# Optimization experiments

Hardware: AMD Instinct MI355X
Metric: run time of the kernel (lower is better)

## Reference

```python
import jax, jax.numpy as jnp
import numpy as np

D_IN = 1024
D_OUT = 1024
CTX_LEN = 2048
BATCH = 4
SEQ = 2048


def setup_inputs() -> dict:
    key = jax.random.key(0)
    kx, kq, kk, kv = jax.random.split(key, 4)
    x = jax.random.normal(kx, (BATCH, SEQ, D_IN), dtype=jnp.float32)
    s = 1.0 / np.sqrt(D_IN)
    # torch nn.Linear weight is (d_out, d_in); store transposed for x @ W
    W_q = jax.random.uniform(kq, (D_IN, D_OUT), dtype=jnp.float32, minval=-s, maxval=s)
    W_k = jax.random.uniform(kk, (D_IN, D_OUT), dtype=jnp.float32, minval=-s, maxval=s)
    W_v = jax.random.uniform(kv, (D_IN, D_OUT), dtype=jnp.float32, minval=-s, maxval=s)
    return {"x": x, "W_q": W_q, "W_k": W_k, "W_v": W_v}


def reference(x, W_q, W_k, W_v):
    b, n, _ = x.shape
    d_out = W_q.shape[1]
    q = x @ W_q            # [b, n, d_out]
    k = x @ W_k
    v = x @ W_v
    scores = jnp.einsum('bqd,bkd->bqk', q, k)  # [b, n, n]
    causal = jnp.triu(jnp.ones((n, n), dtype=bool), k=1)
    scores = jnp.where(causal, -jnp.inf, scores)
    attn = jax.nn.softmax(scores / jnp.sqrt(jnp.float32(d_out)), axis=-1)
    # dropout p=0.0 -> identity
    return jnp.einsum('bqk,bkd->bqd', attn, v)
```

## Files before the change

kernel.cpp:

```cpp
#include <hip/hip_runtime.h>
#include <hip/hip_bf16.h>

#define BATCH 4
#define SEQ   2048
#define DIN   1024
#define DOUT  1024
#define N3    3072
#define MTOT  (BATCH*SEQ)

typedef __hip_bfloat16 bf16;
typedef __attribute__((ext_vector_type(8))) short bf16x8;
typedef __attribute__((ext_vector_type(4))) float f32x4;

#define MFMA(a,b,c) __builtin_amdgcn_mfma_f32_16x16x32_bf16(a,b,c,0,0,0)

union pack4 { bf16 h[4]; uint2 u2; };
union pack8 { bf16 h[8]; bf16x8 v; };

__device__ __forceinline__ void gl16(const bf16* g, bf16* l)
{
    __builtin_amdgcn_global_load_lds(
        (const __attribute__((address_space(1))) void*)g,
        (__attribute__((address_space(3))) void*)l, 16, 0, 0);
}


__global__ __launch_bounds__(256)
void k_prep(const float* __restrict__ x, const float* __restrict__ Wq,
            const float* __restrict__ Wk, const float* __restrict__ Wv,
            bf16* __restrict__ xb, bf16* __restrict__ Wt)
{
    __shared__ bf16 t[64][68];
    const int bid = blockIdx.x;
    if (bid < 8192) {
        long i = ((long)bid * 256 + threadIdx.x) * 4;
        float4 v = *(const float4*)(x + i);
        pack4 o;
        o.h[0] = __float2bfloat16(v.x);
        o.h[1] = __float2bfloat16(v.y);
        o.h[2] = __float2bfloat16(v.z);
        o.h[3] = __float2bfloat16(v.w);
        *(uint2*)(xb + i) = o.u2;
        return;
    }
    const int idx = bid - 8192;
    const int mat = idx >> 8;
    const int rem = idx & 255;
    const int k0 = (rem >> 4) * 64, n0 = (rem & 15) * 64;
    const float* W = (mat == 0) ? Wq : ((mat == 1) ? Wk : Wv);
#pragma unroll
    for (int p = 0; p < 4; ++p) {
        int kr = p * 16 + (threadIdx.x >> 4);
        int c4 = (threadIdx.x & 15) * 4;
        float4 v = *(const float4*)&W[(long)(k0 + kr) * DOUT + n0 + c4];
        t[c4 + 0][kr] = __float2bfloat16(v.x);
        t[c4 + 1][kr] = __float2bfloat16(v.y);
        t[c4 + 2][kr] = __float2bfloat16(v.z);
        t[c4 + 3][kr] = __float2bfloat16(v.w);
    }
    __syncthreads();
    bf16* O = Wt + (long)mat * DIN * DOUT;
#pragma unroll
    for (int i = 0; i < 2; ++i) {
        int l = threadIdx.x + i * 256;
        int n = l >> 3, c8 = (l & 7) * 8;
        pack8 o;
#pragma unroll
        for (int j = 0; j < 8; ++j) o.h[j] = t[n][c8 + j];
        *(bf16x8*)&O[(long)(n0 + n) * DIN + k0 + c8] = o.v;
    }
}


__device__ __forceinline__ void gemm_core(
    const bf16* __restrict__ Ab, long lda,
    const bf16* __restrict__ Bb, long ldb,
    int nk, bf16* __restrict__ As, bf16* __restrict__ Bs,
    f32x4 acc[4][4])
{
    const int tid  = threadIdx.x;
    const int lane = tid & 63;
    const int wave = tid >> 6;
    const int wm = (wave >> 1) * 64;
    const int wn = (wave & 1) * 64;
    const int r  = lane & 15;
    const int qd = lane >> 4;

    const int row0 = tid >> 3;
    const int c    = (tid & 7) ^ (row0 & 7);
    const long aoff = (long)row0 * lda + c * 8;
    const long boff = (long)row0 * ldb + c * 8;
    const long astep = 32 * lda, bstep = 32 * ldb;
    bf16* dA = &As[tid * 8];
    bf16* dB = &Bs[tid * 8];

    for (int kk = 0; kk < nk; ++kk) {
        const bf16* A = Ab + kk * 64 + aoff;
        const bf16* B = Bb + kk * 64 + boff;
#pragma unroll
        for (int i = 0; i < 4; ++i) {
            gl16(A + i * astep, dA + i * 2048);
            gl16(B + i * bstep, dB + i * 2048);
        }
        __syncthreads();
#pragma unroll
        for (int ks = 0; ks < 2; ++ks) {
            const int slot = ((ks * 4 + qd) ^ (r & 7)) * 8;
            bf16x8 af[4], bv[4];
#pragma unroll
            for (int mi = 0; mi < 4; ++mi)
                af[mi] = *(const bf16x8*)&As[(wm + mi * 16 + r) * 64 + slot];
#pragma unroll
            for (int ni = 0; ni < 4; ++ni)
                bv[ni] = *(const bf16x8*)&Bs[(wn + ni * 16 + r) * 64 + slot];
#pragma unroll
            for (int mi = 0; mi < 4; ++mi)
#pragma unroll
                for (int ni = 0; ni < 4; ++ni)
                    acc[mi][ni] = MFMA(af[mi], bv[ni], acc[mi][ni]);
        }
        __syncthreads();
    }
}


__global__ __launch_bounds__(256)
void k_gemm_qkv(const bf16* __restrict__ xb, const bf16* __restrict__ Wt,
                bf16* __restrict__ QK, bf16* __restrict__ Vt)
{
    __shared__ __align__(16) bf16 smem[17408];
    bf16* As = smem;
    bf16* Bs = smem + 8192;
    const int m0 = blockIdx.y * 128, n0 = blockIdx.x * 128;
    f32x4 acc[4][4] = {};
    gemm_core(xb + (long)m0 * DIN, DIN, Wt + (long)n0 * DIN, DIN, DIN / 64, As, Bs, acc);

    const int tid = threadIdx.x;
    const int lane = tid & 63, wave = tid >> 6;
    const int wm = (wave >> 1) * 64, wn = (wave & 1) * 64;
    const int r = lane & 15, qd = lane >> 4;

    if (n0 < 2048) {
#pragma unroll
        for (int mi = 0; mi < 4; ++mi)
#pragma unroll
            for (int ni = 0; ni < 4; ++ni)
#pragma unroll
                for (int j = 0; j < 4; ++j) {
                    int row = m0 + wm + mi * 16 + qd * 4 + j;
                    int col = n0 + wn + ni * 16 + r;
                    QK[(long)row * 2048 + col] = __float2bfloat16(acc[mi][ni][j]);
                }
    } else {
        const int ld = 136;
        bf16* T = smem;
#pragma unroll
        for (int mi = 0; mi < 4; ++mi)
#pragma unroll
            for (int ni = 0; ni < 4; ++ni) {
                pack4 p;
#pragma unroll
                for (int j = 0; j < 4; ++j) p.h[j] = __float2bfloat16(acc[mi][ni][j]);
                int d_l = wn + ni * 16 + r;
                int s_l = wm + mi * 16 + qd * 4;
                *(uint2*)&T[d_l * ld + s_l] = p.u2;
            }
        __syncthreads();
        const int n0v = n0 - 2048;
        const int bb = m0 >> 11;
        const int s0 = m0 & 2047;
        bf16* Ob = Vt + (long)bb * DOUT * SEQ + s0;
#pragma unroll
        for (int p = 0; p < 8; ++p) {
            int l = tid + p * 256;
            int d = l >> 4, s8 = (l & 15) * 8;
            bf16x8 vv = *(const bf16x8*)&T[d * ld + s8];
            *(bf16x8*)&Ob[(long)(n0v + d) * SEQ + s8] = vv;
        }
    }
}


__global__ __launch_bounds__(256, 3)
void k_gemm_scores(const bf16* __restrict__ QK, bf16* __restrict__ P,
                   float* __restrict__ rowSum)
{
    const int b = blockIdx.z, qt = blockIdx.y, kt = blockIdx.x;
    if (kt > qt) return;
    __shared__ __align__(16) bf16 As[128 * 64];
    __shared__ __align__(16) bf16 Bs[128 * 64];
    const bf16* A  = QK + (long)b * SEQ * 2048;
    const bf16* Bt = A + 1024;
    f32x4 acc[4][4] = {};
    gemm_core(A + (long)qt * 128 * 2048, 2048, Bt + (long)kt * 128 * 2048, 2048,
              DIN / 64, As, Bs, acc);

    bf16* Pb = P + (long)b * SEQ * SEQ;
    float* RS = rowSum + b * SEQ;
    const int lane = threadIdx.x & 63, wave = threadIdx.x >> 6;
    const int wm = (wave >> 1) * 64, wn = (wave & 1) * 64;
    const int r = lane & 15, qd = lane >> 4;

    float rp[4][4];
#pragma unroll
    for (int mi = 0; mi < 4; ++mi)
#pragma unroll
        for (int j = 0; j < 4; ++j) rp[mi][j] = 0.f;

#pragma unroll
    for (int mi = 0; mi < 4; ++mi)
#pragma unroll
        for (int ni = 0; ni < 4; ++ni)
#pragma unroll
            for (int j = 0; j < 4; ++j) {
                int row = qt * 128 + wm + mi * 16 + qd * 4 + j;
                int col = kt * 128 + wn + ni * 16 + r;
                float e = (col > row) ? 0.f : __expf(acc[mi][ni][j] * 0.03125f);
                rp[mi][j] += e;
                Pb[(long)row * SEQ + col] = __float2bfloat16(e);
            }
#pragma unroll
    for (int d = 1; d < 16; d <<= 1)
#pragma unroll
        for (int mi = 0; mi < 4; ++mi)
#pragma unroll
            for (int j = 0; j < 4; ++j)
                rp[mi][j] += __shfl_xor(rp[mi][j], d, 64);
    if (r == 0) {
#pragma unroll
        for (int mi = 0; mi < 4; ++mi)
#pragma unroll
            for (int j = 0; j < 4; ++j) {
                int row = qt * 128 + wm + mi * 16 + qd * 4 + j;
                atomicAdd(&RS[row], rp[mi][j]);
            }
    }
}


__global__ __launch_bounds__(256, 3)
void k_gemm_pv(const bf16* __restrict__ P, const bf16* __restrict__ Vt,
               const float* __restrict__ rowSum, float* __restrict__ O)
{
    const int b = blockIdx.z, nt = blockIdx.x;
    const int qt = (SEQ / 128 - 1) - blockIdx.y;
    __shared__ __align__(16) bf16 As[128 * 64];
    __shared__ __align__(16) bf16 Bs[128 * 64];
    const bf16* A  = P + (long)b * SEQ * SEQ + (long)qt * 128 * SEQ;
    const bf16* Bt = Vt + (long)b * DOUT * SEQ;
    const int nk = (qt + 1) * 2;
    f32x4 acc[4][4] = {};
    gemm_core(A, SEQ, Bt + (long)nt * 128 * SEQ, SEQ, nk, As, Bs, acc);

    float* Ob = O + (long)b * SEQ * DOUT;
    const float* RS = rowSum + b * SEQ;
    const int lane = threadIdx.x & 63, wave = threadIdx.x >> 6;
    const int wm = (wave >> 1) * 64, wn = (wave & 1) * 64;
    const int r = lane & 15, qd = lane >> 4;
#pragma unroll
    for (int mi = 0; mi < 4; ++mi)
#pragma unroll
        for (int j = 0; j < 4; ++j) {
            int row = qt * 128 + wm + mi * 16 + qd * 4 + j;
            float inv = 1.0f / RS[row];
#pragma unroll
            for (int ni = 0; ni < 4; ++ni) {
                int col = nt * 128 + wn + ni * 16 + r;
                Ob[(long)row * DOUT + col] = acc[mi][ni][j] * inv;
            }
        }
}


extern "C" void kernel_launch(void* const* d_in, const int* in_sizes, int n_in,
                              void* d_out, int out_size, void* d_ws, size_t ws_size,
                              hipStream_t stream)
{
    const float* x  = (const float*)d_in[0];
    const float* Wq = (const float*)d_in[1];
    const float* Wk = (const float*)d_in[2];
    const float* Wv = (const float*)d_in[3];
    float* out = (float*)d_out;

    char* ws = (char*)d_ws;
    bf16*  xb = (bf16*)(ws);
    bf16*  Wt = (bf16*)(ws + 16777216);
    bf16*  QK = (bf16*)(ws + 23068672);
    bf16*  Vt = (bf16*)(ws + 56623104);
    bf16*  P  = (bf16*)(ws + 73400320);
    float* RS = (float*)(ws + 106954752);

    hipMemsetAsync(RS, 0, BATCH * SEQ * sizeof(float), stream);
    k_prep<<<dim3(8192 + 768), 256, 0, stream>>>(x, Wq, Wk, Wv, xb, Wt);
    k_gemm_qkv<<<dim3(N3 / 128, MTOT / 128), 256, 0, stream>>>(xb, Wt, QK, Vt);
    k_gemm_scores<<<dim3(SEQ / 128, SEQ / 128, BATCH), 256, 0, stream>>>(QK, P, RS);
    k_gemm_pv<<<dim3(DOUT / 128, SEQ / 128, BATCH), 256, 0, stream>>>(P, Vt, RS, out);
}
```

Before: 223.3 us.

## Rewrite QKV projection GEMM as 128x256 tile, 8-wave pipelined kernel

Replaces the QKV GEMM with a 512-thread kernel on 128x256 tiles. It double-buffers LDS with async global-to-LDS loads, interleaved across two half-iterations, and raises wave priority around the MFMA bursts. The aim is to hide global load latency behind MFMA work and halve the number of blocks so each loaded tile is reused more. In exchange it uses about 96KB of LDS per block and hand-tuned vmcnt waits that are fragile if the staging order changes.

```diff
diff --git a/kernel.cpp b/kernel.cpp
--- a/kernel.cpp
+++ b/kernel.cpp
@@ -72,6 +72,150 @@
 }
 
 
+#define BAR() do { __builtin_amdgcn_sched_barrier(0); \
+                   __builtin_amdgcn_s_barrier();      \
+                   __builtin_amdgcn_sched_barrier(0); } while (0)
+
+__global__ __launch_bounds__(512, 2)
+void k_gemm_qkv(const bf16* __restrict__ xb, const bf16* __restrict__ Wt,
+                bf16* __restrict__ QK, bf16* __restrict__ Vt)
+{
+    __shared__ __align__(16) bf16 smem[49152];
+    bf16* sA = smem;
+    bf16* sB = smem + 16384;
+
+    const int tid = threadIdx.x;
+    const int m0 = blockIdx.y * 128;
+    const int n0 = blockIdx.x * 256;
+
+    const bf16* Abase = xb + (long)m0 * DIN;
+    const bf16* Bbase = Wt + (long)n0 * DIN;
+
+    const int srow = tid >> 3;
+    const int scol = ((tid & 7) ^ (srow & 7)) * 8;
+
+    const int lane = tid & 63, wave = tid >> 6;
+    const int wr = wave >> 2, wc = wave & 3;
+    const int r = lane & 15, qd = lane >> 4;
+    const int aRow  = (wr * 64 + r) * 64;
+    const int bHalf = wc >> 1;
+    const int bRow  = ((wc & 1) * 64 + r) * 64;
+    const int slot0 = ( qd      ^ (r & 7)) * 8;
+    const int slot1 = ((4 + qd) ^ (r & 7)) * 8;
+
+    auto stageA = [&](int kt, int pass) {
+        const bf16* src = Abase + (long)(srow + pass * 64) * DIN + kt * 64 + scol;
+        gl16(src, &sA[(kt & 1) * 8192 + pass * 4096 + tid * 8]);
+    };
+    auto stageB = [&](int kt, int half, int pass) {
+        const bf16* src = Bbase + (long)(half * 128 + srow + pass * 64) * DIN + kt * 64 + scol;
+        gl16(src, &sB[(kt & 1) * 16384 + half * 8192 + pass * 4096 + tid * 8]);
+    };
+
+    f32x4 acc[4][4] = {};
+
+    stageB(0, 0, 0); stageB(0, 0, 1); stageB(0, 1, 0); stageB(0, 1, 1);
+    stageA(0, 0);    stageA(0, 1);
+    stageB(1, 0, 0); stageB(1, 0, 1); stageB(1, 1, 0);
+    asm volatile("s_waitcnt vmcnt(3)" ::: "memory");
+    BAR();
+
+#pragma unroll 2
+    for (int kt = 0; kt < 16; ++kt) {
+        const int c = kt & 1;
+        const bf16* A = sA + c * 8192;
+        const bf16* B = sB + c * 16384 + bHalf * 8192;
+
+        bf16x8 bv[4][2], af[2][2];
+#pragma unroll
+        for (int ni = 0; ni < 4; ++ni) {
+            bv[ni][0] = *(const bf16x8*)&B[bRow + ni * 1024 + slot0];
+            bv[ni][1] = *(const bf16x8*)&B[bRow + ni * 1024 + slot1];
+        }
+#pragma unroll
+        for (int mi = 0; mi < 2; ++mi) {
+            af[mi][0] = *(const bf16x8*)&A[aRow + mi * 1024 + slot0];
+            af[mi][1] = *(const bf16x8*)&A[aRow + mi * 1024 + slot1];
+        }
+        if (kt + 1 < 16) { stageB(kt + 1, 1, 1); stageA(kt + 1, 0); stageA(kt + 1, 1); }
+        BAR();
+        asm volatile("s_waitcnt lgkmcnt(0)" ::: "memory");
+        __builtin_amdgcn_s_setprio(1);
+#pragma unroll
+        for (int mi = 0; mi < 2; ++mi)
+#pragma unroll
+            for (int ni = 0; ni < 4; ++ni) {
+                acc[mi][ni] = MFMA(af[mi][0], bv[ni][0], acc[mi][ni]);
+                acc[mi][ni] = MFMA(af[mi][1], bv[ni][1], acc[mi][ni]);
+            }
+        __builtin_amdgcn_s_setprio(0);
+        BAR();
+
+        bf16x8 ag[2][2];
+#pragma unroll
+        for (int mi = 0; mi < 2; ++mi) {
+            ag[mi][0] = *(const bf16x8*)&A[aRow + (mi + 2) * 1024 + slot0];
+            ag[mi][1] = *(const bf16x8*)&A[aRow + (mi + 2) * 1024 + slot1];
+        }
+        if (kt + 2 < 16) { stageB(kt + 2, 0, 0); stageB(kt + 2, 0, 1); stageB(kt + 2, 1, 0); }
+        BAR();
+        asm volatile("s_waitcnt lgkmcnt(0)" ::: "memory");
+        __builtin_amdgcn_s_setprio(1);
+#pragma unroll
+        for (int mi = 0; mi < 2; ++mi)
+#pragma unroll
+            for (int ni = 0; ni < 4; ++ni) {
+                acc[mi + 2][ni] = MFMA(ag[mi][0], bv[ni][0], acc[mi + 2][ni]);
+                acc[mi + 2][ni] = MFMA(ag[mi][1], bv[ni][1], acc[mi + 2][ni]);
+            }
+        __builtin_amdgcn_s_setprio(0);
+        if (kt < 14)       { asm volatile("s_waitcnt vmcnt(3)" ::: "memory"); }
+        else if (kt == 14) { asm volatile("s_waitcnt vmcnt(0)" ::: "memory"); }
+        BAR();
+    }
+
+    const int bx = blockIdx.x;
+    if (bx < 8) {
+#pragma unroll
+        for (int mi = 0; mi < 4; ++mi)
+#pragma unroll
+            for (int ni = 0; ni < 4; ++ni)
+#pragma unroll
+                for (int j = 0; j < 4; ++j) {
+                    int row = m0 + wr * 64 + mi * 16 + qd * 4 + j;
+                    int col = n0 + wc * 64 + ni * 16 + r;
+                    QK[(long)row * 2048 + col] = __float2bfloat16(acc[mi][ni][j]);
+                }
+    } else {
+        const int ld = 136;
+        bf16* T = smem;
+#pragma unroll
+        for (int mi = 0; mi < 4; ++mi)
+#pragma unroll
+            for (int ni = 0; ni < 4; ++ni) {
+                pack4 p;
+#pragma unroll
+                for (int j = 0; j < 4; ++j) p.h[j] = __float2bfloat16(acc[mi][ni][j]);
+                int d_l = wc * 64 + ni * 16 + r;
+                int s_l = wr * 64 + mi * 16 + qd * 4;
+                *(uint2*)&T[d_l * ld + s_l] = p.u2;
+            }
+        __syncthreads();
+        const int n0v = n0 - 2048;
+        const int bb = m0 >> 11;
+        const int s0 = m0 & 2047;
+        bf16* Ob = Vt + (long)bb * DOUT * SEQ + s0;
+#pragma unroll
+        for (int p = 0; p < 8; ++p) {
+            int l = tid + p * 512;
+            int d = l >> 4, s8 = (l & 15) * 8;
+            bf16x8 vv = *(const bf16x8*)&T[d * ld + s8];
+            *(bf16x8*)&Ob[(long)(n0v + d) * SEQ + s8] = vv;
+        }
+    }
+}
+
+
 __device__ __forceinline__ void gemm_core(
     const bf16* __restrict__ Ab, long lda,
     const bf16* __restrict__ Bb, long ldb,
@@ -120,63 +264,6 @@
                     acc[mi][ni] = MFMA(af[mi], bv[ni], acc[mi][ni]);
         }
         __syncthreads();
-    }
-}
-
-
-__global__ __launch_bounds__(256)
-void k_gemm_qkv(const bf16* __restrict__ xb, const bf16* __restrict__ Wt,
-                bf16* __restrict__ QK, bf16* __restrict__ Vt)
-{
-    __shared__ __align__(16) bf16 smem[17408];
-    bf16* As = smem;
-    bf16* Bs = smem + 8192;
-    const int m0 = blockIdx.y * 128, n0 = blockIdx.x * 128;
-    f32x4 acc[4][4] = {};
-    gemm_core(xb + (long)m0 * DIN, DIN, Wt + (long)n0 * DIN, DIN, DIN / 64, As, Bs, acc);
-
-    const int tid = threadIdx.x;
-    const int lane = tid & 63, wave = tid >> 6;
-    const int wm = (wave >> 1) * 64, wn = (wave & 1) * 64;
-    const int r = lane & 15, qd = lane >> 4;
-
-    if (n0 < 2048) {
-#pragma unroll
-        for (int mi = 0; mi < 4; ++mi)
-#pragma unroll
-            for (int ni = 0; ni < 4; ++ni)
-#pragma unroll
-                for (int j = 0; j < 4; ++j) {
-                    int row = m0 + wm + mi * 16 + qd * 4 + j;
-                    int col = n0 + wn + ni * 16 + r;
-                    QK[(long)row * 2048 + col] = __float2bfloat16(acc[mi][ni][j]);
-                }
-    } else {
-        const int ld = 136;
-        bf16* T = smem;
-#pragma unroll
-        for (int mi = 0; mi < 4; ++mi)
-#pragma unroll
-            for (int ni = 0; ni < 4; ++ni) {
-                pack4 p;
-#pragma unroll
-                for (int j = 0; j < 4; ++j) p.h[j] = __float2bfloat16(acc[mi][ni][j]);
-                int d_l = wn + ni * 16 + r;
-                int s_l = wm + mi * 16 + qd * 4;
-                *(uint2*)&T[d_l * ld + s_l] = p.u2;
-            }
-        __syncthreads();
-        const int n0v = n0 - 2048;
-        const int bb = m0 >> 11;
-        const int s0 = m0 & 2047;
-        bf16* Ob = Vt + (long)bb * DOUT * SEQ + s0;
-#pragma unroll
-        for (int p = 0; p < 8; ++p) {
-            int l = tid + p * 256;
-            int d = l >> 4, s8 = (l & 15) * 8;
-            bf16x8 vv = *(const bf16x8*)&T[d * ld + s8];
-            *(bf16x8*)&Ob[(long)(n0v + d) * SEQ + s8] = vv;
-        }
     }
 }
 
@@ -292,7 +379,7 @@
 
     hipMemsetAsync(RS, 0, BATCH * SEQ * sizeof(float), stream);
     k_prep<<<dim3(8192 + 768), 256, 0, stream>>>(x, Wq, Wk, Wv, xb, Wt);
-    k_gemm_qkv<<<dim3(N3 / 128, MTOT / 128), 256, 0, stream>>>(xb, Wt, QK, Vt);
+    k_gemm_qkv<<<dim3(N3 / 256, MTOT / 128), 512, 0, stream>>>(xb, Wt, QK, Vt);
     k_gemm_scores<<<dim3(SEQ / 128, SEQ / 128, BATCH), 256, 0, stream>>>(QK, P, RS);
     k_gemm_pv<<<dim3(DOUT / 128, SEQ / 128, BATCH), 256, 0, stream>>>(P, Vt, RS, out);
 }
```

Result: no change. 222.5 us (-0.4%).

## Rewrite QKV projection GEMM as 256x256 tile ping-pong pipelined kernel

Applied to the files above, without the earlier changes.

Replaces the 128x128 QKV GEMM with a 512-thread, 256x256-tile kernel that double-buffers LDS through direct global-to-LDS loads. It interleaves quarter-tile MFMA blocks with the next tile's loads using explicit barriers, waitcnt and setprio. It also remaps block IDs in an XCD-aware order for L2 locality. The aim is to raise MFMA utilisation and data reuse in the projection, at the cost of 128KB of LDS, heavy register use and fragile hand-written synchronisation.

```diff
diff --git a/kernel.cpp b/kernel.cpp
--- a/kernel.cpp
+++ b/kernel.cpp
@@ -72,6 +72,183 @@
 }
 
 
+#define SBAR() do { __builtin_amdgcn_sched_barrier(0); \
+                    __builtin_amdgcn_s_barrier();      \
+                    __builtin_amdgcn_sched_barrier(0); } while (0)
+
+#define RD_A(Ab, mg) do { _Pragma("unroll")                                    \
+    for (int m_ = 0; m_ < 4; ++m_) {                                           \
+        fa[m_][0] = *(const bf16x8*)&(Ab)[aBase + ((mg)+m_)*1024 + r*64 + slot0]; \
+        fa[m_][1] = *(const bf16x8*)&(Ab)[aBase + ((mg)+m_)*1024 + r*64 + slot1]; \
+    } } while (0)
+
+#define RD_B(Bb, ng) do { _Pragma("unroll")                                    \
+    for (int n_ = 0; n_ < 2; ++n_) {                                           \
+        fb[(ng)+n_][0] = *(const bf16x8*)&(Bb)[bBase + ((ng)+n_)*1024 + r*64 + slot0]; \
+        fb[(ng)+n_][1] = *(const bf16x8*)&(Bb)[bBase + ((ng)+n_)*1024 + r*64 + slot1]; \
+    } } while (0)
+
+#define MFMA_Q(mg, ng) do { __builtin_amdgcn_s_setprio(1);                     \
+    _Pragma("unroll") for (int m_ = 0; m_ < 4; ++m_)                           \
+    _Pragma("unroll") for (int n_ = 0; n_ < 2; ++n_) {                         \
+        acc[(mg)+m_][(ng)+n_] = MFMA(fa[m_][0], fb[(ng)+n_][0], acc[(mg)+m_][(ng)+n_]); \
+        acc[(mg)+m_][(ng)+n_] = MFMA(fa[m_][1], fb[(ng)+n_][1], acc[(mg)+m_][(ng)+n_]); \
+    } __builtin_amdgcn_s_setprio(0); } while (0)
+
+__global__ __launch_bounds__(512, 2)
+void k_gemm_qkv(const bf16* __restrict__ xb, const bf16* __restrict__ Wt,
+                bf16* __restrict__ QK, bf16* __restrict__ Vt)
+{
+    __shared__ __align__(16) bf16 smem[65536];
+    bf16* sA = smem;
+    bf16* sB = smem + 32768;
+
+    const int tid = threadIdx.x;
+    const int wg  = blockIdx.y * 12 + blockIdx.x;
+    const int swz = (wg & 7) * 48 + (wg >> 3);
+    const int bx  = swz % 12, by = swz / 12;
+    const int m0 = by * 256, n0 = bx * 256;
+
+    const bf16* Ag = xb + (long)m0 * DIN;
+    const bf16* Bg = Wt + (long)n0 * DIN;
+
+    const int srow = tid >> 3;
+    const int scol = ((tid & 7) ^ (srow & 7)) * 8;
+
+    const int lane = tid & 63, wave = tid >> 6;
+    const int wr = wave >> 2, wc = wave & 3;
+    const int r = lane & 15, qd = lane >> 4;
+    const int aBase = (wr * 128) * 64;
+    const int bBase = (wc * 64) * 64;
+    const int slot0 = ( qd      ^ (r & 7)) * 8;
+    const int slot1 = ((4 + qd) ^ (r & 7)) * 8;
+
+    auto stA = [&](int t, int h, int p) {
+        const bf16* src = Ag + (long)(h * 128 + p * 64 + srow) * DIN + t * 64 + scol;
+        gl16(src, &sA[(t & 1) * 16384 + h * 8192 + p * 4096 + tid * 8]);
+    };
+    auto stB = [&](int t, int h, int p) {
+        const bf16* src = Bg + (long)(h * 128 + p * 64 + srow) * DIN + t * 64 + scol;
+        gl16(src, &sB[(t & 1) * 16384 + h * 8192 + p * 4096 + tid * 8]);
+    };
+
+    f32x4 acc[8][4] = {};
+    bf16x8 fa[4][2], fb[4][2];
+
+    stB(0,0,0); stB(0,0,1); stB(0,1,0); stB(0,1,1);
+    stA(0,0,0); stA(0,0,1); stA(0,1,0); stA(0,1,1);
+    stB(1,0,0); stB(1,0,1); stB(1,1,0); stB(1,1,1);
+    asm volatile("s_waitcnt vmcnt(4)" ::: "memory");
+    SBAR();
+
+#pragma unroll 1
+    for (int i = 0; i < 8; ++i) {
+        const int e = 2 * i, o = e + 1;
+        const bf16* A0 = sA;
+        const bf16* B0 = sB;
+        const bf16* A1 = sA + 16384;
+        const bf16* B1 = sB + 16384;
+        const bool more = (i < 7);
+
+        RD_A(A0, 0); RD_B(B0, 0);
+        stA(o, 0, 0); stA(o, 0, 1);
+        SBAR();
+        MFMA_Q(0, 0);
+        SBAR();
+
+        RD_B(B0, 2);
+        stA(o, 1, 0); stA(o, 1, 1);
+        SBAR();
+        MFMA_Q(0, 2);
+        SBAR();
+
+        RD_A(A0, 4);
+        if (more) { stB(e + 2, 0, 0); stB(e + 2, 0, 1); }
+        SBAR();
+        MFMA_Q(4, 0);
+        SBAR();
+
+        if (more) { stB(e + 2, 1, 0); stB(e + 2, 1, 1); }
+        SBAR();
+        MFMA_Q(4, 2);
+        __builtin_amdgcn_sched_barrier(0);
+        if (more) { asm volatile("s_waitcnt vmcnt(4)" ::: "memory"); }
+        else      { asm volatile("s_waitcnt vmcnt(0)" ::: "memory"); }
+        SBAR();
+
+        RD_A(A1, 0); RD_B(B1, 0);
+        if (more) { stA(e + 2, 0, 0); stA(e + 2, 0, 1); }
+        SBAR();
+        MFMA_Q(0, 0);
+        SBAR();
+
+        RD_B(B1, 2);
+        if (more) { stA(e + 2, 1, 0); stA(e + 2, 1, 1); }
+        SBAR();
+        MFMA_Q(0, 2);
+        SBAR();
+
+        RD_A(A1, 4);
+        if (more) { stB(o + 2, 0, 0); stB(o + 2, 0, 1); }
+        SBAR();
+        MFMA_Q(4, 0);
+        SBAR();
+
+        if (more) { stB(o + 2, 1, 0); stB(o + 2, 1, 1); }
+        SBAR();
+        MFMA_Q(4, 2);
+        __builtin_amdgcn_sched_barrier(0);
+        if (more) { asm volatile("s_waitcnt vmcnt(4)" ::: "memory"); }
+        SBAR();
+    }
+
+    if (bx < 8) {
+#pragma unroll
+        for (int mi = 0; mi < 8; ++mi)
+#pragma unroll
+            for (int ni = 0; ni < 4; ++ni)
+#pragma unroll
+                for (int j = 0; j < 4; ++j) {
+                    int row = m0 + wr * 128 + mi * 16 + qd * 4 + j;
+                    int col = n0 + wc * 64 + ni * 16 + r;
+                    QK[(long)row * 2048 + col] = __float2bfloat16(acc[mi][ni][j]);
+                }
+    } else {
+        const int ld = 136;
+        bf16* T = smem;
+        const int n0v = n0 - 2048;
+        const int bb = m0 >> 11;
+        const int s0 = m0 & 2047;
+        bf16* Ob = Vt + (long)bb * DOUT * SEQ + s0;
+#pragma unroll
+        for (int h = 0; h < 2; ++h) {
+            if (h) __syncthreads();
+            if (wr == h) {
+#pragma unroll
+                for (int mi = 0; mi < 8; ++mi)
+#pragma unroll
+                    for (int ni = 0; ni < 4; ++ni) {
+                        pack4 p;
+#pragma unroll
+                        for (int j = 0; j < 4; ++j) p.h[j] = __float2bfloat16(acc[mi][ni][j]);
+                        int d_l = wc * 64 + ni * 16 + r;
+                        int s_l = mi * 16 + qd * 4;
+                        *(uint2*)&T[d_l * ld + s_l] = p.u2;
+                    }
+            }
+            __syncthreads();
+#pragma unroll
+            for (int p = 0; p < 8; ++p) {
+                int l = tid + p * 512;
+                int d = l >> 4, s8 = (l & 15) * 8;
+                bf16x8 vv = *(const bf16x8*)&T[d * ld + s8];
+                *(bf16x8*)&Ob[(long)(n0v + d) * SEQ + s0 * 0 + h * 128 + s8] = vv;
+            }
+        }
+    }
+}
+
+
 __device__ __forceinline__ void gemm_core(
     const bf16* __restrict__ Ab, long lda,
     const bf16* __restrict__ Bb, long ldb,
@@ -120,63 +297,6 @@
                     acc[mi][ni] = MFMA(af[mi], bv[ni], acc[mi][ni]);
         }
         __syncthreads();
-    }
-}
-
-
-__global__ __launch_bounds__(256)
-void k_gemm_qkv(const bf16* __restrict__ xb, const bf16* __restrict__ Wt,
-                bf16* __restrict__ QK, bf16* __restrict__ Vt)
-{
-    __shared__ __align__(16) bf16 smem[17408];
-    bf16* As = smem;
-    bf16* Bs = smem + 8192;
-    const int m0 = blockIdx.y * 128, n0 = blockIdx.x * 128;
-    f32x4 acc[4][4] = {};
-    gemm_core(xb + (long)m0 * DIN, DIN, Wt + (long)n0 * DIN, DIN, DIN / 64, As, Bs, acc);
-
-    const int tid = threadIdx.x;
-    const int lane = tid & 63, wave = tid >> 6;
-    const int wm = (wave >> 1) * 64, wn = (wave & 1) * 64;
-    const int r = lane & 15, qd = lane >> 4;
-
-    if (n0 < 2048) {
-#pragma unroll
-        for (int mi = 0; mi < 4; ++mi)
-#pragma unroll
-            for (int ni = 0; ni < 4; ++ni)
-#pragma unroll
-                for (int j = 0; j < 4; ++j) {
-                    int row = m0 + wm + mi * 16 + qd * 4 + j;
-                    int col = n0 + wn + ni * 16 + r;
-                    QK[(long)row * 2048 + col] = __float2bfloat16(acc[mi][ni][j]);
-                }
-    } else {
-        const int ld = 136;
-        bf16* T = smem;
-#pragma unroll
-        for (int mi = 0; mi < 4; ++mi)
-#pragma unroll
-            for (int ni = 0; ni < 4; ++ni) {
-                pack4 p;
-#pragma unroll
-                for (int j = 0; j < 4; ++j) p.h[j] = __float2bfloat16(acc[mi][ni][j]);
-                int d_l = wn + ni * 16 + r;
-                int s_l = wm + mi * 16 + qd * 4;
-                *(uint2*)&T[d_l * ld + s_l] = p.u2;
-            }
-        __syncthreads();
-        const int n0v = n0 - 2048;
-        const int bb = m0 >> 11;
-        const int s0 = m0 & 2047;
-        bf16* Ob = Vt + (long)bb * DOUT * SEQ + s0;
-#pragma unroll
-        for (int p = 0; p < 8; ++p) {
-            int l = tid + p * 256;
-            int d = l >> 4, s8 = (l & 15) * 8;
-            bf16x8 vv = *(const bf16x8*)&T[d * ld + s8];
-            *(bf16x8*)&Ob[(long)(n0v + d) * SEQ + s8] = vv;
-        }
     }
 }
 
@@ -292,7 +412,7 @@
 
     hipMemsetAsync(RS, 0, BATCH * SEQ * sizeof(float), stream);
     k_prep<<<dim3(8192 + 768), 256, 0, stream>>>(x, Wq, Wk, Wv, xb, Wt);
-    k_gemm_qkv<<<dim3(N3 / 128, MTOT / 128), 256, 0, stream>>>(xb, Wt, QK, Vt);
+    k_gemm_qkv<<<dim3(12, 32), 512, 0, stream>>>(xb, Wt, QK, Vt);
     k_gemm_scores<<<dim3(SEQ / 128, SEQ / 128, BATCH), 256, 0, stream>>>(QK, P, RS);
     k_gemm_pv<<<dim3(DOUT / 128, SEQ / 128, BATCH), 256, 0, stream>>>(P, Vt, RS, out);
 }
```

After: 228.2 us. 2.2% more time.

## Stage score tile in LDS for coalesced P stores and compact triangular grid

Applied to the files above, without the earlier changes.

The scores kernel now writes its exponentiated tile into shared memory and then stores it to global as 16-byte vectors, replacing the scattered 2-byte stores. Its grid becomes a flat 1D list of only the 544 lower-triangular tiles, so blocks that would exit immediately are no longer launched. The PV kernel also switches to a 1D grid ordered longest-first, with batch and column tiles interleaved. The cost is a larger LDS footprint, an extra barrier, and a small loop to decode the tile index.

```diff
diff --git a/kernel.cpp b/kernel.cpp
--- a/kernel.cpp
+++ b/kernel.cpp
@@ -185,10 +185,16 @@
 void k_gemm_scores(const bf16* __restrict__ QK, bf16* __restrict__ P,
                    float* __restrict__ rowSum)
 {
-    const int b = blockIdx.z, qt = blockIdx.y, kt = blockIdx.x;
-    if (kt > qt) return;
-    __shared__ __align__(16) bf16 As[128 * 64];
-    __shared__ __align__(16) bf16 Bs[128 * 64];
+    const int bid = blockIdx.x;
+    const int b = bid & 3;
+    int rem = bid >> 2;
+    int qt = 15;
+    while (rem > qt) { rem -= (qt + 1); --qt; }
+    const int kt = rem;
+
+    __shared__ __align__(16) bf16 smem[17408];
+    bf16* As = smem;
+    bf16* Bs = smem + 8192;
     const bf16* A  = QK + (long)b * SEQ * 2048;
     const bf16* Bt = A + 1024;
     f32x4 acc[4][4] = {};
@@ -197,10 +203,14 @@
 
     bf16* Pb = P + (long)b * SEQ * SEQ;
     float* RS = rowSum + b * SEQ;
-    const int lane = threadIdx.x & 63, wave = threadIdx.x >> 6;
+    const int tid = threadIdx.x;
+    const int lane = tid & 63, wave = tid >> 6;
     const int wm = (wave >> 1) * 64, wn = (wave & 1) * 64;
     const int r = lane & 15, qd = lane >> 4;
 
+    const int ld = 136;
+    bf16* T = smem;
+
     float rp[4][4];
 #pragma unroll
     for (int mi = 0; mi < 4; ++mi)
@@ -213,11 +223,13 @@
         for (int ni = 0; ni < 4; ++ni)
 #pragma unroll
             for (int j = 0; j < 4; ++j) {
-                int row = qt * 128 + wm + mi * 16 + qd * 4 + j;
-                int col = kt * 128 + wn + ni * 16 + r;
+                int row_l = wm + mi * 16 + qd * 4 + j;
+                int col_l = wn + ni * 16 + r;
+                int row = qt * 128 + row_l;
+                int col = kt * 128 + col_l;
                 float e = (col > row) ? 0.f : __expf(acc[mi][ni][j] * 0.03125f);
                 rp[mi][j] += e;
-                Pb[(long)row * SEQ + col] = __float2bfloat16(e);
+                T[row_l * ld + col_l] = __float2bfloat16(e);
             }
 #pragma unroll
     for (int d = 1; d < 16; d <<= 1)
@@ -235,6 +247,14 @@
                 atomicAdd(&RS[row], rp[mi][j]);
             }
     }
+    __syncthreads();
+#pragma unroll
+    for (int p = 0; p < 8; ++p) {
+        int l = tid + p * 256;
+        int row_l = l >> 4, c8 = (l & 15) * 8;
+        bf16x8 vv = *(const bf16x8*)&T[row_l * ld + c8];
+        *(bf16x8*)&Pb[(long)(qt * 128 + row_l) * SEQ + kt * 128 + c8] = vv;
+    }
 }
 
 
@@ -242,8 +262,10 @@
 void k_gemm_pv(const bf16* __restrict__ P, const bf16* __restrict__ Vt,
                const float* __restrict__ rowSum, float* __restrict__ O)
 {
-    const int b = blockIdx.z, nt = blockIdx.x;
-    const int qt = (SEQ / 128 - 1) - blockIdx.y;
+    const int bid = blockIdx.x;
+    const int qt = 15 - (bid >> 5);
+    const int b  = (bid >> 3) & 3;
+    const int nt = bid & 7;
     __shared__ __align__(16) bf16 As[128 * 64];
     __shared__ __align__(16) bf16 Bs[128 * 64];
     const bf16* A  = P + (long)b * SEQ * SEQ + (long)qt * 128 * SEQ;
@@ -293,6 +315,6 @@
     hipMemsetAsync(RS, 0, BATCH * SEQ * sizeof(float), stream);
     k_prep<<<dim3(8192 + 768), 256, 0, stream>>>(x, Wq, Wk, Wv, xb, Wt);
     k_gemm_qkv<<<dim3(N3 / 128, MTOT / 128), 256, 0, stream>>>(xb, Wt, QK, Vt);
-    k_gemm_scores<<<dim3(SEQ / 128, SEQ / 128, BATCH), 256, 0, stream>>>(QK, P, RS);
-    k_gemm_pv<<<dim3(DOUT / 128, SEQ / 128, BATCH), 256, 0, stream>>>(P, Vt, RS, out);
-}
+    k_gemm_scores<<<dim3(544), 256, 0, stream>>>(QK, P, RS);
+    k_gemm_pv<<<dim3(512), 256, 0, stream>>>(P, Vt, RS, out);
+}
```

After: 217.0 us. 2.9% less time.
